# Kernel tuning notes

Hardware: AMD Instinct MI355X
Metric: run time of the kernel (lower is better)

Reference implementation:

```python
import jax, jax.numpy as jnp
import numpy as np

G = 64          # grid_size
BC = 16         # base_channels
LATENT = 128

def _conv3d_s2(x, w, b):
    # x: [B,C,D,H,W], w: [O,I,3,3,3], stride 2, pad 1
    y = jax.lax.conv_general_dilated(
        x, w, window_strides=(2, 2, 2), padding=((1, 1), (1, 1), (1, 1)),
        dimension_numbers=('NCDHW', 'OIDHW', 'NCDHW'))
    return y + b[None, :, None, None, None]

def setup_inputs() -> dict:
    key = jax.random.key(0)
    ks = jax.random.split(key, 9)
    B, N = 32, 16384
    partial_coords = jax.random.uniform(ks[0], (B, N, 3), jnp.float32, -1.0, 1.0)
    def he(k, shape, fan_in):
        return jax.random.normal(k, shape, jnp.float32) * np.float32(np.sqrt(2.0 / fan_in))
    w1 = he(ks[1], (BC, 1, 3, 3, 3), 1 * 27)
    b1 = jnp.zeros((BC,), jnp.float32)
    w2 = he(ks[2], (2 * BC, BC, 3, 3, 3), BC * 27)
    b2 = jnp.zeros((2 * BC,), jnp.float32)
    w3 = he(ks[3], (4 * BC, 2 * BC, 3, 3, 3), 2 * BC * 27)
    b3 = jnp.zeros((4 * BC,), jnp.float32)
    fc_in = 4 * BC * (G // 8) ** 3
    fc_w = he(ks[4], (LATENT, fc_in), fc_in)
    fc_b = jnp.zeros((LATENT,), jnp.float32)
    return {'partial_coords': partial_coords, 'w1': w1, 'b1': b1, 'w2': w2,
            'b2': b2, 'w3': w3, 'b3': b3, 'fc_w': fc_w, 'fc_b': fc_b}

def reference(partial_coords, w1, b1, w2, b2, w3, b3, fc_w, fc_b):
    B, N, _ = partial_coords.shape
    # voxelize: scale [-1,1] -> [0, G-1], truncate (matches torch .long()), clamp
    coords_scaled = (partial_coords + 1.0) * 0.5 * (G - 1)
    ci = jnp.clip(coords_scaled.astype(jnp.int32), 0, G - 1)  # [B,N,3] = (x,y,z)
    bidx = jnp.broadcast_to(jnp.arange(B, dtype=jnp.int32)[:, None], (B, N))
    grid = jnp.zeros((B, G, G, G), jnp.float32)
    # grid[b, z, y, x] = 1.0  (single vectorized scatter)
    grid = grid.at[bidx, ci[..., 2], ci[..., 1], ci[..., 0]].set(1.0)
    x = grid[:, None]  # [B,1,G,G,G]
    x = jax.nn.relu(_conv3d_s2(x, w1, b1))
    x = jax.nn.relu(_conv3d_s2(x, w2, b2))
    x = jax.nn.relu(_conv3d_s2(x, w3, b3))  # [B,4*BC,G/8,G/8,G/8]
    feat = x.reshape(B, -1)
    return feat @ fc_w.T + fc_b  # [B,128]
```

## Files before the change

kernel.cpp:

```cpp
#include <hip/hip_runtime.h>
#include <hip/hip_bf16.h>


typedef __attribute__((ext_vector_type(8))) short bf16x8;
typedef __attribute__((ext_vector_type(4))) float f32x4;

__device__ inline unsigned short f2bf(float f) {
    __hip_bfloat16 h = __float2bfloat16(f);
    return *reinterpret_cast<unsigned short*>(&h);
}

__global__ void k_scatter(const float* __restrict__ coords,
                          unsigned char* __restrict__ grid) {
    int i = blockIdx.x * 256 + threadIdx.x;
    float cx = coords[3 * i + 0];
    float cy = coords[3 * i + 1];
    float cz = coords[3 * i + 2];
    int ix = (int)((cx + 1.0f) * 0.5f * 63.0f);
    int iy = (int)((cy + 1.0f) * 0.5f * 63.0f);
    int iz = (int)((cz + 1.0f) * 0.5f * 63.0f);
    ix = min(max(ix, 0), 63);
    iy = min(max(iy, 0), 63);
    iz = min(max(iz, 0), 63);
    int b = i >> 14;
    grid[((b * 64 + iz) * 64 + iy) * 64 + ix] = 1;
}

__global__ void k_conv1(const unsigned char* __restrict__ grid,
                        const float* __restrict__ w1,
                        const float* __restrict__ b1,
                        unsigned short* __restrict__ c1b) {
    int idx = blockIdx.x * 256 + threadIdx.x;
    int x = idx & 31, y = (idx >> 5) & 31, z = (idx >> 10) & 31, b = idx >> 15;
    const unsigned char* g = grid + b * 262144;
    float in27[27];
#pragma unroll
    for (int kz = 0; kz < 3; ++kz)
#pragma unroll
        for (int ky = 0; ky < 3; ++ky)
#pragma unroll
            for (int kx = 0; kx < 3; ++kx) {
                int iz = 2 * z + kz - 1, iy = 2 * y + ky - 1, ix = 2 * x + kx - 1;
                bool ok = ((unsigned)iz < 64u) & ((unsigned)iy < 64u) & ((unsigned)ix < 64u);
                in27[kz * 9 + ky * 3 + kx] = ok ? (float)g[(iz * 64 + iy) * 64 + ix] : 0.0f;
            }
    float r[16];
#pragma unroll
    for (int oc = 0; oc < 16; ++oc) {
        float acc = b1[oc];
#pragma unroll
        for (int k = 0; k < 27; ++k) acc = fmaf(w1[oc * 27 + k], in27[k], acc);
        r[oc] = fmaxf(acc, 0.0f);
    }
    unsigned int dw[8];
#pragma unroll
    for (int j = 0; j < 8; ++j)
        dw[j] = (unsigned int)f2bf(r[2 * j]) | ((unsigned int)f2bf(r[2 * j + 1]) << 16);
    char* base = (char*)c1b + (size_t)idx * 32;
    *(int4*)base        = int4{(int)dw[0], (int)dw[1], (int)dw[2], (int)dw[3]};
    *(int4*)(base + 16) = int4{(int)dw[4], (int)dw[5], (int)dw[6], (int)dw[7]};
}

__global__ void k_wtrans(const float* __restrict__ w2, unsigned short* __restrict__ w2b,
                         const float* __restrict__ w3, unsigned short* __restrict__ w3b) {
    int i = blockIdx.x * 256 + threadIdx.x;
    if (i < 14336) {
        int sh = i >> 9, oc = (i >> 4) & 31, c = i & 15;
        float v = (sh < 27) ? w2[oc * 432 + c * 27 + sh] : 0.0f;
        w2b[i] = f2bf(v);
    } else {
        int j = i - 14336;
        if (j < 55296) {
            int sh = j >> 11, oc = (j >> 5) & 63, c = j & 31;
            w3b[j] = f2bf(w3[oc * 864 + c * 27 + sh]);
        }
    }
}

__device__ constexpr int abase(int sh) {
    return (sh / 9) * 35376 + (((sh % 9) / 3) & 1) * 18224 +
           (((sh % 9) / 3) >> 1) * 1072 + (sh % 3) * 32;
}

__global__ __launch_bounds__(512) void k_conv2_mfma(
        const unsigned short* __restrict__ c1b,
        const unsigned short* __restrict__ w2b,
        const float* __restrict__ b2,
        unsigned short* __restrict__ c2b) {
    __shared__ __align__(16) char smem[106128];
    const int t = threadIdx.x;
    const int b = blockIdx.x >> 4;
    const int zo = blockIdx.x & 15;
    const int lane = t & 63;
    const int wid = t >> 6;

    {
        const int4 z4 = {0, 0, 0, 0};
        if (t < 198) {
            int p = t / 66, r = t % 66;
            int col = r >> 1, h = r & 1;
            *(int4*)(smem + p * 35376 + col * 32 + h * 16) = z4;
        }
        if (t >= 256 && t < 454) {
            int i = t - 256;
            int p = i / 66, r = i % 66;
            int row33 = r >> 1, h = r & 1;
            int off = (row33 < 17) ? row33 * 1072 : 18224 + (row33 - 17) * 1072;
            *(int4*)(smem + p * 35376 + off + h * 16) = z4;
        }
    }

    const char* src = (const char*)c1b + (size_t)b * (32768 * 32);
#pragma unroll
    for (int i = 0; i < 6; ++i) {
        const int p = i >> 1;
        int pos = ((i & 1) << 9) + t;
        int iy = pos >> 5, ix = pos & 31;
        int iz = 2 * zo + p - 1;
        int4 v0 = {0, 0, 0, 0}, v1 = {0, 0, 0, 0};
        if (iz >= 0) {
            const char* gp = src + ((size_t)(iz * 1024 + pos)) * 32;
            v0 = *(const int4*)gp;
            v1 = *(const int4*)(gp + 16);
        }
        int iy_st = iy + 1;
        char* d = smem + p * 35376 + ((iy_st & 1) ? 18224 : 0) + (iy_st >> 1) * 1072 +
                  (ix + 1) * 32;
        *(int4*)d = v0;
        *(int4*)(d + 16) = v1;
    }
    __syncthreads();

    const int y = lane & 15;
    const int g = lane >> 4;
    const int h = g & 1;
    const int s = g >> 1;
    const int laneA = y * 1072 + h * 16;
    const int laneB = (lane & 15) * 32 + h * 16 + s * 1024;
    const int x0 = wid * 2;
    const char* wbase = (const char*)w2b;

    f32x4 acc00 = {0, 0, 0, 0}, acc01 = {0, 0, 0, 0};
    f32x4 acc10 = {0, 0, 0, 0}, acc11 = {0, 0, 0, 0};

#pragma unroll
    for (int sp = 0; sp < 14; ++sp) {
        const int sh0 = 2 * sp;
        const int sh1 = (2 * sp + 1 < 27) ? 2 * sp + 1 : 26;
        const int a0 = abase(sh0);
        const int d01 = abase(sh1) - a0;
        const int addrA = laneA + a0 + (s ? d01 : 0) + x0 * 64;
        bf16x8 A0 = *(const bf16x8*)(smem + addrA);
        bf16x8 A1 = *(const bf16x8*)(smem + addrA + 64);
        const char* wb = wbase + sp * 2048 + laneB;
        bf16x8 B0 = *(const bf16x8*)wb;
        bf16x8 B1 = *(const bf16x8*)(wb + 512);
        acc00 = __builtin_amdgcn_mfma_f32_16x16x32_bf16(A0, B0, acc00, 0, 0, 0);
        acc01 = __builtin_amdgcn_mfma_f32_16x16x32_bf16(A0, B1, acc01, 0, 0, 0);
        acc10 = __builtin_amdgcn_mfma_f32_16x16x32_bf16(A1, B0, acc10, 0, 0, 0);
        acc11 = __builtin_amdgcn_mfma_f32_16x16x32_bf16(A1, B1, acc11, 0, 0, 0);
    }

    __syncthreads();
    float* sOut = (float*)smem;
    {
        int ocl = lane & 15;
        int yb = (lane >> 4) * 4;
#pragma unroll
        for (int r = 0; r < 4; ++r) {
            sOut[ocl * 257        + (yb + r) * 16 + x0    ] = acc00[r];
            sOut[(ocl + 16) * 257 + (yb + r) * 16 + x0    ] = acc01[r];
            sOut[ocl * 257        + (yb + r) * 16 + x0 + 1] = acc10[r];
            sOut[(ocl + 16) * 257 + (yb + r) * 16 + x0 + 1] = acc11[r];
        }
    }
    __syncthreads();
    {
        int m = t >> 1, half = t & 1;
        unsigned int dw[8];
#pragma unroll
        for (int j = 0; j < 8; ++j) {
            int oc0 = half * 16 + 2 * j;
            float v0 = fmaxf(sOut[oc0 * 257 + m] + b2[oc0], 0.0f);
            float v1 = fmaxf(sOut[(oc0 + 1) * 257 + m] + b2[oc0 + 1], 0.0f);
            dw[j] = (unsigned int)f2bf(v0) | ((unsigned int)f2bf(v1) << 16);
        }
        char* dst = (char*)c2b + ((size_t)b * 4096 + zo * 256 + m) * 64 + half * 32;
        *(int4*)dst        = int4{(int)dw[0], (int)dw[1], (int)dw[2], (int)dw[3]};
        *(int4*)(dst + 16) = int4{(int)dw[4], (int)dw[5], (int)dw[6], (int)dw[7]};
    }
}

__global__ __launch_bounds__(512) void k_conv3_mfma(
        const unsigned short* __restrict__ c2b,
        const unsigned short* __restrict__ w3b,
        const float* __restrict__ b3,
        float* __restrict__ feat) {
    __shared__ __align__(16) char smem[55488];
    const int t = threadIdx.x;
    const int b = blockIdx.x >> 3;
    const int zo = blockIdx.x & 7;
    const int lane = t & 63;
    const int wid = t >> 6;

    if (t < 396) {
        int p3 = t / 132, j = t % 132;
        int v = j >> 2, g = j & 3;
        int iy_st = (v < 17) ? 0 : (v - 16);
        int ix_st = (v < 17) ? v : 0;
        int ux = (ix_st & 1) ? 9 + (ix_st >> 1) : (ix_st >> 1);
        int u = (p3 * 17 + iy_st) * 17 + ux;
        *(int4*)(smem + u * 64 + g * 16) = int4{0, 0, 0, 0};
    }

    const char* src = (const char*)c2b + (size_t)b * 262144;
#pragma unroll
    for (int r = 0; r < 6; ++r) {
        int i = r * 512 + t;
        int g = i & 3, vox = i >> 2;
        int kz = vox >> 8, pos = vox & 255;
        int iy = pos >> 4, ix = pos & 15;
        int iz = 2 * zo + kz - 1;
        int4 v = {0, 0, 0, 0};
        if (iz >= 0)
            v = *(const int4*)(src + ((size_t)(iz * 256 + pos)) * 64 + g * 16);
        int ix_st = ix + 1;
        int ux = (ix_st & 1) ? 9 + (ix_st >> 1) : (ix_st >> 1);
        int u = (kz * 17 + iy + 1) * 17 + ux;
        *(int4*)(smem + u * 64 + g * 16) = v;
    }
    __syncthreads();

    const int mt = wid >> 1;
    const int ntp = wid & 1;
    const int m = mt * 16 + (lane & 15);
    const int y = m >> 3, x = m & 7;
    const int g = lane >> 4;
    const int laneA = (34 * y + x) * 64 + g * 16;
    const char* wb_base = (const char*)w3b + (ntp * 32 + (lane & 15)) * 64 + g * 16;

    f32x4 acc0 = {0, 0, 0, 0}, acc1 = {0, 0, 0, 0};

#pragma unroll
    for (int sh = 0; sh < 27; ++sh) {
        const int kz = sh / 9, ky = (sh % 9) / 3, kx = sh % 3;
        const int uxc = (kx == 0) ? 0 : ((kx == 1) ? 9 : 1);
        const int aoff = (289 * kz + 17 * ky + uxc) * 64;
        bf16x8 A = *(const bf16x8*)(smem + laneA + aoff);
        const char* wb = wb_base + sh * 4096;
        bf16x8 B0 = *(const bf16x8*)wb;
        bf16x8 B1 = *(const bf16x8*)(wb + 1024);
        acc0 = __builtin_amdgcn_mfma_f32_16x16x32_bf16(A, B0, acc0, 0, 0, 0);
        acc1 = __builtin_amdgcn_mfma_f32_16x16x32_bf16(A, B1, acc1, 0, 0, 0);
    }

    __syncthreads();
    float* sOut = (float*)smem;
    {
        int ocl = lane & 15;
        int mb = mt * 16 + (lane >> 4) * 4;
#pragma unroll
        for (int r = 0; r < 4; ++r) {
            sOut[(ntp * 32 + ocl) * 65 + mb + r]      = acc0[r];
            sOut[(ntp * 32 + 16 + ocl) * 65 + mb + r] = acc1[r];
        }
    }
    __syncthreads();
    {
        int oc = t >> 3, q = t & 7;
        float bb = b3[oc];
        float* dst = feat + (size_t)b * 32768 + oc * 512 + zo * 64 + q * 8;
#pragma unroll
        for (int k = 0; k < 8; ++k) {
            float v = sOut[oc * 65 + q * 8 + k] + bb;
            dst[k] = fmaxf(v, 0.0f);
        }
    }
}

__global__ void k_fc(const float* __restrict__ feat,
                     const float* __restrict__ fc_w,
                     const float* __restrict__ fc_b,
                     float* __restrict__ out) {
    __shared__ float lds[256 * 36];
    int fchunk = blockIdx.x & 127;
    int lg = blockIdx.x >> 7;
    int t = threadIdx.x;
    int f0 = fchunk * 256;
    for (int b = 0; b < 32; ++b)
        lds[t * 36 + b] = feat[b * 32768 + f0 + t];
    __syncthreads();

    int l = lg * 32 + (t >> 3);
    int bq = t & 7;
    const float* wrow = fc_w + l * 32768 + f0;
    float a0 = 0.f, a1 = 0.f, a2 = 0.f, a3 = 0.f;
    for (int f = 0; f < 256; ++f) {
        float wv = wrow[f];
        const float* p = &lds[f * 36 + bq * 4];
        a0 = fmaf(p[0], wv, a0);
        a1 = fmaf(p[1], wv, a1);
        a2 = fmaf(p[2], wv, a2);
        a3 = fmaf(p[3], wv, a3);
    }
    if (fchunk == 0) {
        float bb = fc_b[l];
        a0 += bb; a1 += bb; a2 += bb; a3 += bb;
    }
    int b0 = bq * 4;
    atomicAdd(&out[(b0 + 0) * 128 + l], a0);
    atomicAdd(&out[(b0 + 1) * 128 + l], a1);
    atomicAdd(&out[(b0 + 2) * 128 + l], a2);
    atomicAdd(&out[(b0 + 3) * 128 + l], a3);
}

extern "C" void kernel_launch(void* const* d_in, const int* in_sizes, int n_in,
                              void* d_out, int out_size, void* d_ws, size_t ws_size,
                              hipStream_t stream) {
    const float* coords = (const float*)d_in[0];
    const float* w1 = (const float*)d_in[1];
    const float* b1 = (const float*)d_in[2];
    const float* w2 = (const float*)d_in[3];
    const float* b2 = (const float*)d_in[4];
    const float* w3 = (const float*)d_in[5];
    const float* b3 = (const float*)d_in[6];
    const float* fc_w = (const float*)d_in[7];
    const float* fc_b = (const float*)d_in[8];

    unsigned char* grid_u8 = (unsigned char*)d_ws;
    unsigned short* w2b = (unsigned short*)((char*)d_ws + 65536);
    unsigned short* w3b = (unsigned short*)((char*)d_ws + 131072);
    unsigned short* c1b = (unsigned short*)((char*)d_ws + 8388608);
    unsigned short* c2b = (unsigned short*)((char*)d_ws + 75497472);
    float* feat = (float*)((char*)d_ws + 92274688);
    float* out = (float*)d_out;

    hipMemsetAsync(grid_u8, 0, 8388608, stream);
    hipMemsetAsync(out, 0, 32 * 128 * sizeof(float), stream);

    k_scatter<<<2048, 256, 0, stream>>>(coords, grid_u8);
    k_conv1<<<4096, 256, 0, stream>>>(grid_u8, w1, b1, c1b);
    k_wtrans<<<272, 256, 0, stream>>>(w2, w2b, w3, w3b);
    k_conv2_mfma<<<512, 512, 0, stream>>>(c1b, w2b, b2, c2b);
    k_conv3_mfma<<<256, 512, 0, stream>>>(c2b, w3b, b3, feat);
    k_fc<<<512, 256, 0, stream>>>(feat, fc_w, fc_b, out);
}
```

Baseline: 165.9 us.

## Stage conv1 input halo in LDS and replace FC atomics with two-pass reduction

conv1 now assigns each block an 8x8x4 output tile. The block loads the matching 9x17x17 input halo from the byte grid into LDS once, splitting odd and even x columns so the stride-2 reads come from contiguous locations, and each thread takes its 27 taps from LDS instead of global memory. The FC stage no longer uses float atomics and the output memset. Partial sums are written to a workspace buffer and a small second kernel adds the 128 chunks plus the bias. This removes atomic contention and makes the sum order deterministic, at the cost of one extra launch and a 2 MB partial buffer.

```diff
diff --git a/kernel.cpp b/kernel.cpp
--- a/kernel.cpp
+++ b/kernel.cpp
@@ -26,13 +26,34 @@
     grid[((b * 64 + iz) * 64 + iy) * 64 + ix] = 1;
 }
 
-__global__ void k_conv1(const unsigned char* __restrict__ grid,
-                        const float* __restrict__ w1,
-                        const float* __restrict__ b1,
-                        unsigned short* __restrict__ c1b) {
-    int idx = blockIdx.x * 256 + threadIdx.x;
-    int x = idx & 31, y = (idx >> 5) & 31, z = (idx >> 10) & 31, b = idx >> 15;
+__global__ __launch_bounds__(256) void k_conv1(
+        const unsigned char* __restrict__ grid,
+        const float* __restrict__ w1,
+        const float* __restrict__ b1,
+        unsigned short* __restrict__ c1b) {
+    __shared__ float hal[9 * 17 * 20];
+    const int t = threadIdx.x;
+    const int blk = blockIdx.x;
+    const int b = blk >> 7;
+    const int zb = (blk >> 4) & 7;
+    const int yb = (blk >> 2) & 3;
+    const int xb = blk & 3;
+    const int iz0 = 8 * zb - 1, iy0 = 16 * yb - 1, ix0 = 16 * xb - 1;
+
     const unsigned char* g = grid + b * 262144;
+    for (int i = t; i < 2601; i += 256) {
+        int hz = i / 289, rm = i - hz * 289;
+        int hy = rm / 17, hx = rm - hy * 17;
+        int iz = iz0 + hz, iy = iy0 + hy, ix = ix0 + hx;
+        bool ok = (iz >= 0) & (iy >= 0) & (ix >= 0);
+        float v = ok ? (float)g[(iz * 64 + iy) * 64 + ix] : 0.0f;
+        int ux = (hx & 1) ? 10 + (hx >> 1) : (hx >> 1);
+        hal[(hz * 17 + hy) * 20 + ux] = v;
+    }
+    __syncthreads();
+
+    const int x = t & 7, y = (t >> 3) & 7, tz = t >> 6;
+    const int base = (2 * tz * 17) * 20 + (2 * y) * 20 + x;
     float in27[27];
 #pragma unroll
     for (int kz = 0; kz < 3; ++kz)
@@ -40,9 +61,9 @@
         for (int ky = 0; ky < 3; ++ky)
 #pragma unroll
             for (int kx = 0; kx < 3; ++kx) {
-                int iz = 2 * z + kz - 1, iy = 2 * y + ky - 1, ix = 2 * x + kx - 1;
-                bool ok = ((unsigned)iz < 64u) & ((unsigned)iy < 64u) & ((unsigned)ix < 64u);
-                in27[kz * 9 + ky * 3 + kx] = ok ? (float)g[(iz * 64 + iy) * 64 + ix] : 0.0f;
+                int uxo = (kx == 1) ? 10 : ((kx == 2) ? 1 : 0);
+                in27[kz * 9 + ky * 3 + kx] =
+                    hal[base + (kz * 17 + ky) * 20 + uxo];
             }
     float r[16];
 #pragma unroll
@@ -56,9 +77,11 @@
 #pragma unroll
     for (int j = 0; j < 8; ++j)
         dw[j] = (unsigned int)f2bf(r[2 * j]) | ((unsigned int)f2bf(r[2 * j + 1]) << 16);
-    char* base = (char*)c1b + (size_t)idx * 32;
-    *(int4*)base        = int4{(int)dw[0], (int)dw[1], (int)dw[2], (int)dw[3]};
-    *(int4*)(base + 16) = int4{(int)dw[4], (int)dw[5], (int)dw[6], (int)dw[7]};
+    int oz = 4 * zb + tz, oy = 8 * yb + y, ox = 8 * xb + x;
+    size_t idx = ((size_t)(b * 32 + oz) * 32 + oy) * 32 + ox;
+    char* base_o = (char*)c1b + idx * 32;
+    *(int4*)base_o        = int4{(int)dw[0], (int)dw[1], (int)dw[2], (int)dw[3]};
+    *(int4*)(base_o + 16) = int4{(int)dw[4], (int)dw[5], (int)dw[6], (int)dw[7]};
 }
 
 __global__ void k_wtrans(const float* __restrict__ w2, unsigned short* __restrict__ w2b,
@@ -278,10 +301,9 @@
     }
 }
 
-__global__ void k_fc(const float* __restrict__ feat,
-                     const float* __restrict__ fc_w,
-                     const float* __restrict__ fc_b,
-                     float* __restrict__ out) {
+__global__ void k_fc_partial(const float* __restrict__ feat,
+                             const float* __restrict__ fc_w,
+                             float* __restrict__ part) {
     __shared__ float lds[256 * 36];
     int fchunk = blockIdx.x & 127;
     int lg = blockIdx.x >> 7;
@@ -303,15 +325,24 @@
         a2 = fmaf(p[2], wv, a2);
         a3 = fmaf(p[3], wv, a3);
     }
-    if (fchunk == 0) {
-        float bb = fc_b[l];
-        a0 += bb; a1 += bb; a2 += bb; a3 += bb;
-    }
     int b0 = bq * 4;
-    atomicAdd(&out[(b0 + 0) * 128 + l], a0);
-    atomicAdd(&out[(b0 + 1) * 128 + l], a1);
-    atomicAdd(&out[(b0 + 2) * 128 + l], a2);
-    atomicAdd(&out[(b0 + 3) * 128 + l], a3);
+    float* pd = part + (size_t)fchunk * 4096 + l;
+    pd[(b0 + 0) * 128] = a0;
+    pd[(b0 + 1) * 128] = a1;
+    pd[(b0 + 2) * 128] = a2;
+    pd[(b0 + 3) * 128] = a3;
+}
+
+__global__ void k_fc_reduce(const float* __restrict__ part,
+                            const float* __restrict__ fc_b,
+                            float* __restrict__ out) {
+    int idx = blockIdx.x * 256 + threadIdx.x;
+    int l = idx & 127;
+    float s = fc_b[l];
+#pragma unroll 8
+    for (int fc = 0; fc < 128; ++fc)
+        s += part[fc * 4096 + idx];
+    out[idx] = s;
 }
 
 extern "C" void kernel_launch(void* const* d_in, const int* in_sizes, int n_in,
@@ -333,15 +364,16 @@
     unsigned short* c1b = (unsigned short*)((char*)d_ws + 8388608);
     unsigned short* c2b = (unsigned short*)((char*)d_ws + 75497472);
     float* feat = (float*)((char*)d_ws + 92274688);
+    float* part = (float*)((char*)d_ws + 96468992);
     float* out = (float*)d_out;
 
     hipMemsetAsync(grid_u8, 0, 8388608, stream);
-    hipMemsetAsync(out, 0, 32 * 128 * sizeof(float), stream);
 
     k_scatter<<<2048, 256, 0, stream>>>(coords, grid_u8);
     k_conv1<<<4096, 256, 0, stream>>>(grid_u8, w1, b1, c1b);
     k_wtrans<<<272, 256, 0, stream>>>(w2, w2b, w3, w3b);
     k_conv2_mfma<<<512, 512, 0, stream>>>(c1b, w2b, b2, c2b);
     k_conv3_mfma<<<256, 512, 0, stream>>>(c2b, w3b, b3, feat);
-    k_fc<<<512, 256, 0, stream>>>(feat, fc_w, fc_b, out);
-}
+    k_fc_partial<<<512, 256, 0, stream>>>(feat, fc_w, part);
+    k_fc_reduce<<<16, 256, 0, stream>>>(part, fc_b, out);
+}
```

After: 169.2 us. 2.0% more time.
